# Kernel tuning notes

Hardware: AMD Instinct MI355X
Metric: run time of the kernel (lower is better)

The kernel has to match this reference:

```python
import jax, jax.numpy as jnp
import numpy as np
from math import sqrt

B, S, D, H = 2, 2048, 1024, 16
HD = D // H


def setup_inputs() -> dict:
    key = jax.random.key(0)
    ks = jax.random.split(key, 5)
    std = 0.02
    return {
        "tensor_in": jax.random.normal(ks[0], (B, S, D), dtype=jnp.float32),
        "attention_mask": jnp.zeros((1, 1, S, S), dtype=jnp.float32),
        "Wq": jax.random.normal(ks[1], (D, D), dtype=jnp.float32) * std,
        "Wk": jax.random.normal(ks[2], (D, D), dtype=jnp.float32) * std,
        "Wv": jax.random.normal(ks[3], (D, D), dtype=jnp.float32) * std,
        "Wo": jax.random.normal(ks[4], (D, D), dtype=jnp.float32) * std,
    }


def reference(tensor_in, attention_mask, Wq, Wk, Wv, Wo):
    # nn.Linear(dim, dim, bias=False): y = x @ W.T, W is [out, in]
    q = tensor_in @ Wq.T  # [B,S,D]
    k = tensor_in @ Wk.T
    v = tensor_in @ Wv.T
    # split heads -> [B,H,S,HD]
    q = q.reshape(B, S, H, HD).transpose(0, 2, 1, 3)
    k = k.reshape(B, S, H, HD).transpose(0, 2, 1, 3)
    v = v.reshape(B, S, H, HD).transpose(0, 2, 1, 3)
    # scores [B,H,S,S]; note: mask added BEFORE scaling, scale = sqrt(full dim)
    scores = jnp.einsum("bhqd,bhkd->bhqk", q, k) + attention_mask
    weights = jax.nn.softmax(scores / sqrt(D), axis=-1)  # dropout = identity (eval)
    context = jnp.einsum("bhqk,bhkd->bhqd", weights, v)
    context = context.transpose(0, 2, 1, 3).reshape(B, S, D)
    return context @ Wo.T
```

## Files before the change

kernel.cpp:

```cpp
#include <hip/hip_runtime.h>

#define B_  2
#define S_  2048
#define D_  1024
#define H_  16
#define HD_ 64
#define M_  (B_*S_)

typedef __attribute__((ext_vector_type(8))) short  short8;
typedef __attribute__((ext_vector_type(4))) float  float4v;
typedef __attribute__((ext_vector_type(4))) int    int4v;

#define PSCALE 0.0450843341f

__device__ __forceinline__ unsigned int pack2_bf16(float a, float b) {
#if __has_builtin(__builtin_amdgcn_cvt_pk_bf16_f32)
    auto p = __builtin_amdgcn_cvt_pk_bf16_f32(a, b);
    return __builtin_bit_cast(unsigned int, p);
#else
    unsigned int xa = __builtin_bit_cast(unsigned int, a);
    unsigned int xb = __builtin_bit_cast(unsigned int, b);
    xa += 0x7fffu + ((xa >> 16) & 1u);
    xb += 0x7fffu + ((xb >> 16) & 1u);
    return (xa >> 16) | (xb & 0xffff0000u);
#endif
}
__device__ __forceinline__ unsigned short f_to_bf16bits(float f) {
#if __has_builtin(__builtin_amdgcn_cvt_pk_bf16_f32)
    return (unsigned short)(pack2_bf16(f, f) & 0xffffu);
#else
    unsigned int x = __builtin_bit_cast(unsigned int, f);
    x += 0x7fffu + ((x >> 16) & 1u);
    return (unsigned short)(x >> 16);
#endif
}

__device__ __forceinline__ float fast_exp2(float x) {
#if __has_builtin(__builtin_amdgcn_exp2f)
    return __builtin_amdgcn_exp2f(x);
#else
    return exp2f(x);
#endif
}

__device__ __forceinline__ void async_cp16(const unsigned short* gsrc,
                                           unsigned short* lds_base_uniform) {
#if __has_builtin(__builtin_amdgcn_global_load_lds)
    __builtin_amdgcn_global_load_lds(
        (const __attribute__((address_space(1))) unsigned int*)gsrc,
        (__attribute__((address_space(3))) unsigned int*)lds_base_uniform,
        16, 0, 0);
#else
    const int lane = (int)(threadIdx.x & 63);
    *(int4v*)(lds_base_uniform + lane * 8) = *(const int4v*)gsrc;
#endif
}

__global__ __launch_bounds__(256) void cvt_bf16(
    const float* __restrict__ X,  const float* __restrict__ Wq,
    const float* __restrict__ Wk, const float* __restrict__ Wv,
    const float* __restrict__ Wo,
    unsigned short* __restrict__ Xb,  unsigned short* __restrict__ Wqb,
    unsigned short* __restrict__ Wkb, unsigned short* __restrict__ Wvb,
    unsigned short* __restrict__ Wob)
{
    const long t = (long)blockIdx.x * 256 + threadIdx.x;
    const long e = t * 8;
    const float* src; unsigned short* dst; long off;
    if      (e < 4194304) { src = X;  dst = Xb;  off = e; }
    else if (e < 5242880) { src = Wq; dst = Wqb; off = e - 4194304; }
    else if (e < 6291456) { src = Wk; dst = Wkb; off = e - 5242880; }
    else if (e < 7340032) { src = Wv; dst = Wvb; off = e - 6291456; }
    else                  { src = Wo; dst = Wob; off = e - 7340032; }
    float4v a = *(const float4v*)&src[off];
    float4v b = *(const float4v*)&src[off + 4];
    int4v o;
    o[0] = (int)pack2_bf16(a[0], a[1]);
    o[1] = (int)pack2_bf16(a[2], a[3]);
    o[2] = (int)pack2_bf16(b[0], b[1]);
    o[3] = (int)pack2_bf16(b[2], b[3]);
    *(int4v*)&dst[off] = o;
}

__global__ __launch_bounds__(256) void gemm_bt(
    const unsigned short* __restrict__ A,
    const unsigned short* __restrict__ B0,
    const unsigned short* __restrict__ B1,
    const unsigned short* __restrict__ B2,
    void* __restrict__ O0, void* __restrict__ O1, void* __restrict__ O2,
    int mode_base)
{
    const int K = 1024;
    const int z = blockIdx.z;
    const int mode = mode_base + z;
    const unsigned short* Aop;
    const unsigned short* Bop;
    void* Op = (z == 0) ? O0 : (z == 1) ? O1 : O2;
    int m0, n0;
    if (mode == 2) {
        Aop = B2; Bop = A;
        m0 = blockIdx.y * 128;
        n0 = blockIdx.x * 128;
    } else {
        Aop = A;
        Bop = (z == 0) ? B0 : (z == 1) ? B1 : B2;
        m0 = blockIdx.x * 128;
        n0 = blockIdx.y * 128;
    }

    __shared__ alignas(16) unsigned short As[128 * 64];
    __shared__ alignas(16) unsigned short Bs[128 * 64];

    const int tid  = threadIdx.x;
    const int wv   = tid >> 6;
    const int lane = tid & 63;
    const int wm   = wv >> 1, wn = wv & 1;
    const int q4   = lane >> 4, l15 = lane & 15;

    const unsigned short* gA[4];
    const unsigned short* gB[4];
    unsigned short* ldsA[4];
    unsigned short* ldsB[4];
#pragma unroll
    for (int j = 0; j < 4; j++) {
        const int r = wv * 32 + j * 8 + (lane >> 3);
        const int c = (((lane & 7) ^ (r & 7)) * 8);
        gA[j] = Aop + (long)(m0 + r) * K + c;
        gB[j] = Bop + (long)(n0 + r) * K + c;
        ldsA[j] = &As[(wv * 32 + j * 8) * 64];
        ldsB[j] = &Bs[(wv * 32 + j * 8) * 64];
    }

    int aoff[2][4], boff[2][4];
#pragma unroll
    for (int ks = 0; ks < 2; ks++)
#pragma unroll
        for (int t = 0; t < 4; t++) {
            const int swz = (((ks * 4 + q4) ^ (l15 & 7)) * 8);
            aoff[ks][t] = (wm * 64 + t * 16 + l15) * 64 + swz;
            boff[ks][t] = (wn * 64 + t * 16 + l15) * 64 + swz;
        }

    float4v acc[4][4];
#pragma unroll
    for (int i = 0; i < 4; i++)
#pragma unroll
        for (int j = 0; j < 4; j++) acc[i][j] = (float4v)0.0f;

    for (int k0 = 0; k0 < K; k0 += 64) {
        __syncthreads();
#pragma unroll
        for (int j = 0; j < 4; j++) {
            async_cp16(gA[j], ldsA[j]);
            async_cp16(gB[j], ldsB[j]);
            gA[j] += 64; gB[j] += 64;
        }
        __syncthreads();

#pragma unroll
        for (int ks = 0; ks < 2; ks++) {
            short8 afr[4], bfr[4];
#pragma unroll
            for (int mt = 0; mt < 4; mt++) afr[mt] = *(const short8*)&As[aoff[ks][mt]];
#pragma unroll
            for (int nt = 0; nt < 4; nt++) bfr[nt] = *(const short8*)&Bs[boff[ks][nt]];
#pragma unroll
            for (int mt = 0; mt < 4; mt++)
#pragma unroll
                for (int nt = 0; nt < 4; nt++)
                    acc[mt][nt] = __builtin_amdgcn_mfma_f32_16x16x32_bf16(
                        afr[mt], bfr[nt], acc[mt][nt], 0, 0, 0);
        }
    }

#pragma unroll
    for (int mt = 0; mt < 4; mt++)
#pragma unroll
        for (int nt = 0; nt < 4; nt++)
#pragma unroll
            for (int r = 0; r < 4; r++) {
                const int m = m0 + wm * 64 + mt * 16 + q4 * 4 + r;
                const int n = n0 + wn * 64 + nt * 16 + l15;
                float v = acc[mt][nt][r];
                if (mode == 3) {
                    ((float*)Op)[(long)m * D_ + n] = v;
                } else if (mode == 2) {
                    const long off = (((long)(n >> 11) * H_ + (m >> 6)) * HD_ + (m & 63)) * S_ + (n & 2047);
                    ((unsigned short*)Op)[off] = f_to_bf16bits(v);
                } else {
                    const long off = ((long)((m >> 11) * H_ + (n >> 6)) * S_ + (m & 2047)) * HD_ + (n & 63);
                    if (mode == 0) v *= PSCALE;
                    ((unsigned short*)Op)[off] = f_to_bf16bits(v);
                }
            }
}

__global__ __launch_bounds__(256) void attn(
    const unsigned short* __restrict__ Q,
    const unsigned short* __restrict__ Kk,
    const unsigned short* __restrict__ Vt,
    const float* __restrict__ mask,
    unsigned short* __restrict__ ctx)
{
    __shared__ alignas(16) unsigned short Ks [2][64 * 72];
    __shared__ alignas(16) unsigned short Vts[2][64 * 72];
    __shared__ alignas(16) unsigned short Ps [4][32 * 72];

    const int tid  = threadIdx.x;
    const int wv   = tid >> 6;
    const int lane = tid & 63;
    const int q4   = lane >> 4, l15 = lane & 15;
    const int bh   = blockIdx.y;
    const int q0   = blockIdx.x * 128;

    const long head = (long)bh * S_ * HD_;

    short8 qfr[2][2];
#pragma unroll
    for (int mt = 0; mt < 2; mt++) {
        const int qrow = q0 + wv * 32 + mt * 16 + l15;
        qfr[mt][0] = *(const short8*)&Q[head + (long)qrow * HD_ + q4 * 8];
        qfr[mt][1] = *(const short8*)&Q[head + (long)qrow * HD_ + 32 + q4 * 8];
    }

    float l_acc[2][4];
#pragma unroll
    for (int mt = 0; mt < 2; mt++)
#pragma unroll
        for (int r = 0; r < 4; r++) l_acc[mt][r] = 0.0f;
    float4v oacc[2][4];
#pragma unroll
    for (int mt = 0; mt < 2; mt++)
#pragma unroll
        for (int dt = 0; dt < 4; dt++) oacc[mt][dt] = (float4v)0.0f;

    const int srow = tid >> 3;
    const int scol = (tid & 7) * 8;
    const unsigned short* gK[2];
    const unsigned short* gV[2];
    int ldsOff[2];
#pragma unroll
    for (int j = 0; j < 2; j++) {
        const int row = j * 32 + srow;
        gK[j] = Kk + head + (long)row * HD_ + scol;
        gV[j] = Vt + head + (long)row * S_  + scol;
        ldsOff[j] = row * 72 + scol;
    }

    const float* mrow[2][4];
#pragma unroll
    for (int mt = 0; mt < 2; mt++)
#pragma unroll
        for (int r = 0; r < 4; r++)
            mrow[mt][r] = mask + (long)(q0 + wv * 32 + mt * 16 + q4 * 4 + r) * S_ + l15;

    int4v kreg[2], vreg[2];
#pragma unroll
    for (int j = 0; j < 2; j++) {
        kreg[j] = *(const int4v*)gK[j];
        vreg[j] = *(const int4v*)gV[j];
    }

    for (int it = 0; it < S_ / 64; it++) {
        const int k0  = it * 64;
        const int buf = it & 1;

#pragma unroll
        for (int j = 0; j < 2; j++) {
            *(int4v*)&Ks [buf][ldsOff[j]] = kreg[j];
            *(int4v*)&Vts[buf][ldsOff[j]] = vreg[j];
        }
        __syncthreads();

        if (it + 1 < S_ / 64) {
#pragma unroll
            for (int j = 0; j < 2; j++) {
                kreg[j] = *(const int4v*)(gK[j] + (long)(k0 + 64) * HD_);
                vreg[j] = *(const int4v*)(gV[j] + (k0 + 64));
            }
        }

        float mv[2][4][4];
#pragma unroll
        for (int mt = 0; mt < 2; mt++)
#pragma unroll
            for (int nt = 0; nt < 4; nt++)
#pragma unroll
                for (int r = 0; r < 4; r++)
                    mv[mt][nt][r] = mrow[mt][r][k0 + nt * 16];

        float4v sfr[2][4];
#pragma unroll
        for (int nt = 0; nt < 4; nt++) {
            short8 kb0 = *(const short8*)&Ks[buf][(nt * 16 + l15) * 72 + q4 * 8];
            short8 kb1 = *(const short8*)&Ks[buf][(nt * 16 + l15) * 72 + 32 + q4 * 8];
#pragma unroll
            for (int mt = 0; mt < 2; mt++) {
                float4v s = (float4v)0.0f;
                s = __builtin_amdgcn_mfma_f32_16x16x32_bf16(qfr[mt][0], kb0, s, 0, 0, 0);
                s = __builtin_amdgcn_mfma_f32_16x16x32_bf16(qfr[mt][1], kb1, s, 0, 0, 0);
                sfr[mt][nt] = s;
            }
        }

#pragma unroll
        for (int mt = 0; mt < 2; mt++)
#pragma unroll
            for (int nt = 0; nt < 4; nt++)
#pragma unroll
                for (int r = 0; r < 4; r++) {
                    const float p = fast_exp2(fmaf(mv[mt][nt][r], PSCALE, sfr[mt][nt][r]));
                    l_acc[mt][r] += p;
                    Ps[wv][(mt * 16 + q4 * 4 + r) * 72 + nt * 16 + l15] = f_to_bf16bits(p);
                }

        short8 pf[2][2];
#pragma unroll
        for (int mt = 0; mt < 2; mt++) {
            pf[mt][0] = *(const short8*)&Ps[wv][(mt * 16 + l15) * 72 + q4 * 8];
            pf[mt][1] = *(const short8*)&Ps[wv][(mt * 16 + l15) * 72 + 32 + q4 * 8];
        }

#pragma unroll
        for (int dt = 0; dt < 4; dt++) {
            short8 vb0 = *(const short8*)&Vts[buf][(dt * 16 + l15) * 72 + q4 * 8];
            short8 vb1 = *(const short8*)&Vts[buf][(dt * 16 + l15) * 72 + 32 + q4 * 8];
#pragma unroll
            for (int mt = 0; mt < 2; mt++) {
                float4v o = oacc[mt][dt];
                o = __builtin_amdgcn_mfma_f32_16x16x32_bf16(pf[mt][0], vb0, o, 0, 0, 0);
                o = __builtin_amdgcn_mfma_f32_16x16x32_bf16(pf[mt][1], vb1, o, 0, 0, 0);
                oacc[mt][dt] = o;
            }
        }
    }

#pragma unroll
    for (int mt = 0; mt < 2; mt++)
#pragma unroll
        for (int r = 0; r < 4; r++) {
#pragma unroll
            for (int off = 1; off < 16; off <<= 1)
                l_acc[mt][r] += __shfl_xor(l_acc[mt][r], off);
        }

    const int b = bh >> 4, h = bh & 15;
#pragma unroll
    for (int mt = 0; mt < 2; mt++)
#pragma unroll
        for (int dt = 0; dt < 4; dt++)
#pragma unroll
            for (int r = 0; r < 4; r++) {
                const int qg = q0 + wv * 32 + mt * 16 + q4 * 4 + r;
                const int d  = dt * 16 + l15;
                const float v = oacc[mt][dt][r] / l_acc[mt][r];
                ctx[((long)(b * S_ + qg)) * D_ + h * HD_ + d] = f_to_bf16bits(v);
            }
}

extern "C" void kernel_launch(void* const* d_in, const int* in_sizes, int n_in,
                              void* d_out, int out_size, void* d_ws, size_t ws_size,
                              hipStream_t stream) {
    const float* X    = (const float*)d_in[0];
    const float* mask = (const float*)d_in[1];
    const float* Wq   = (const float*)d_in[2];
    const float* Wk   = (const float*)d_in[3];
    const float* Wv   = (const float*)d_in[4];
    const float* Wo   = (const float*)d_in[5];
    float* out        = (float*)d_out;

    unsigned short* ws = (unsigned short*)d_ws;
    unsigned short* qws  = ws;
    unsigned short* kws  = ws + 4194304;
    unsigned short* vtws = ws + 8388608;
    unsigned short* ctx  = ws + 12582912;
    unsigned short* Xb   = ws + 16777216;
    unsigned short* Wqb  = ws + 20971520;
    unsigned short* Wkb  = ws + 22020096;
    unsigned short* Wvb  = ws + 23068672;
    unsigned short* Wob  = ws + 24117248;

    cvt_bf16<<<dim3(4096), 256, 0, stream>>>(X, Wq, Wk, Wv, Wo, Xb, Wqb, Wkb, Wvb, Wob);
    gemm_bt<<<dim3(32, 8, 3), 256, 0, stream>>>(Xb, Wqb, Wkb, Wvb, qws, kws, vtws, 0);
    attn<<<dim3(16, 32, 1), 256, 0, stream>>>(qws, kws, vtws, mask, ctx);
    gemm_bt<<<dim3(32, 8, 1), 256, 0, stream>>>(ctx, Wob, Wob, Wob, out, out, out, 3);
}
```

Measured before the change: 231.8 us.

## Split attention query tile across eight waves of 16 rows each

The attention kernel now launches 512 threads per block. Each of eight waves owns 16 query rows instead of four waves owning 32 rows. The per-thread K/V staging load drops to one vector per tile and register pressure halves, aiming for higher occupancy and more latency hiding. In exchange each wave reuses every K/V LDS fragment for only one row tile, which doubles LDS reads per MFMA, and block-wide syncs now cover more waves.

```diff
diff --git a/kernel.cpp b/kernel.cpp
--- a/kernel.cpp
+++ b/kernel.cpp
@@ -195,7 +195,7 @@
             }
 }
 
-__global__ __launch_bounds__(256) void attn(
+__global__ __launch_bounds__(512, 4) void attn(
     const unsigned short* __restrict__ Q,
     const unsigned short* __restrict__ Kk,
     const unsigned short* __restrict__ Vt,
@@ -204,7 +204,7 @@
 {
     __shared__ alignas(16) unsigned short Ks [2][64 * 72];
     __shared__ alignas(16) unsigned short Vts[2][64 * 72];
-    __shared__ alignas(16) unsigned short Ps [4][32 * 72];
+    __shared__ alignas(16) unsigned short Ps [8][16 * 72];
 
     const int tid  = threadIdx.x;
     const int wv   = tid >> 6;
@@ -215,147 +215,101 @@
 
     const long head = (long)bh * S_ * HD_;
 
-    short8 qfr[2][2];
-#pragma unroll
-    for (int mt = 0; mt < 2; mt++) {
-        const int qrow = q0 + wv * 32 + mt * 16 + l15;
-        qfr[mt][0] = *(const short8*)&Q[head + (long)qrow * HD_ + q4 * 8];
-        qfr[mt][1] = *(const short8*)&Q[head + (long)qrow * HD_ + 32 + q4 * 8];
-    }
-
-    float l_acc[2][4];
-#pragma unroll
-    for (int mt = 0; mt < 2; mt++)
-#pragma unroll
-        for (int r = 0; r < 4; r++) l_acc[mt][r] = 0.0f;
-    float4v oacc[2][4];
-#pragma unroll
-    for (int mt = 0; mt < 2; mt++)
-#pragma unroll
-        for (int dt = 0; dt < 4; dt++) oacc[mt][dt] = (float4v)0.0f;
+    const int qrow = q0 + wv * 16 + l15;
+    short8 qfr[2];
+    qfr[0] = *(const short8*)&Q[head + (long)qrow * HD_ + q4 * 8];
+    qfr[1] = *(const short8*)&Q[head + (long)qrow * HD_ + 32 + q4 * 8];
+
+    float l_acc[4] = {0.0f, 0.0f, 0.0f, 0.0f};
+    float4v oacc[4];
+#pragma unroll
+    for (int dt = 0; dt < 4; dt++) oacc[dt] = (float4v)0.0f;
 
     const int srow = tid >> 3;
     const int scol = (tid & 7) * 8;
-    const unsigned short* gK[2];
-    const unsigned short* gV[2];
-    int ldsOff[2];
-#pragma unroll
-    for (int j = 0; j < 2; j++) {
-        const int row = j * 32 + srow;
-        gK[j] = Kk + head + (long)row * HD_ + scol;
-        gV[j] = Vt + head + (long)row * S_  + scol;
-        ldsOff[j] = row * 72 + scol;
-    }
-
-    const float* mrow[2][4];
-#pragma unroll
-    for (int mt = 0; mt < 2; mt++)
-#pragma unroll
-        for (int r = 0; r < 4; r++)
-            mrow[mt][r] = mask + (long)(q0 + wv * 32 + mt * 16 + q4 * 4 + r) * S_ + l15;
-
-    int4v kreg[2], vreg[2];
-#pragma unroll
-    for (int j = 0; j < 2; j++) {
-        kreg[j] = *(const int4v*)gK[j];
-        vreg[j] = *(const int4v*)gV[j];
-    }
+    const unsigned short* gK = Kk + head + (long)srow * HD_ + scol;
+    const unsigned short* gV = Vt + head + (long)srow * S_  + scol;
+    const int ldsOff = srow * 72 + scol;
+
+    const float* mrow[4];
+#pragma unroll
+    for (int r = 0; r < 4; r++)
+        mrow[r] = mask + (long)(q0 + wv * 16 + q4 * 4 + r) * S_ + l15;
+
+    int4v kreg = *(const int4v*)gK;
+    int4v vreg = *(const int4v*)gV;
 
     for (int it = 0; it < S_ / 64; it++) {
         const int k0  = it * 64;
         const int buf = it & 1;
 
-#pragma unroll
-        for (int j = 0; j < 2; j++) {
-            *(int4v*)&Ks [buf][ldsOff[j]] = kreg[j];
-            *(int4v*)&Vts[buf][ldsOff[j]] = vreg[j];
-        }
+        *(int4v*)&Ks [buf][ldsOff] = kreg;
+        *(int4v*)&Vts[buf][ldsOff] = vreg;
         __syncthreads();
 
         if (it + 1 < S_ / 64) {
-#pragma unroll
-            for (int j = 0; j < 2; j++) {
-                kreg[j] = *(const int4v*)(gK[j] + (long)(k0 + 64) * HD_);
-                vreg[j] = *(const int4v*)(gV[j] + (k0 + 64));
-            }
-        }
-
-        float mv[2][4][4];
-#pragma unroll
-        for (int mt = 0; mt < 2; mt++)
-#pragma unroll
-            for (int nt = 0; nt < 4; nt++)
-#pragma unroll
-                for (int r = 0; r < 4; r++)
-                    mv[mt][nt][r] = mrow[mt][r][k0 + nt * 16];
-
-        float4v sfr[2][4];
+            kreg = *(const int4v*)(gK + (long)(k0 + 64) * HD_);
+            vreg = *(const int4v*)(gV + (k0 + 64));
+        }
+
+        float mv[4][4];
+#pragma unroll
+        for (int nt = 0; nt < 4; nt++)
+#pragma unroll
+            for (int r = 0; r < 4; r++)
+                mv[nt][r] = mrow[r][k0 + nt * 16];
+
+        float4v sfr[4];
 #pragma unroll
         for (int nt = 0; nt < 4; nt++) {
             short8 kb0 = *(const short8*)&Ks[buf][(nt * 16 + l15) * 72 + q4 * 8];
             short8 kb1 = *(const short8*)&Ks[buf][(nt * 16 + l15) * 72 + 32 + q4 * 8];
-#pragma unroll
-            for (int mt = 0; mt < 2; mt++) {
-                float4v s = (float4v)0.0f;
-                s = __builtin_amdgcn_mfma_f32_16x16x32_bf16(qfr[mt][0], kb0, s, 0, 0, 0);
-                s = __builtin_amdgcn_mfma_f32_16x16x32_bf16(qfr[mt][1], kb1, s, 0, 0, 0);
-                sfr[mt][nt] = s;
+            float4v s = (float4v)0.0f;
+            s = __builtin_amdgcn_mfma_f32_16x16x32_bf16(qfr[0], kb0, s, 0, 0, 0);
+            s = __builtin_amdgcn_mfma_f32_16x16x32_bf16(qfr[1], kb1, s, 0, 0, 0);
+            sfr[nt] = s;
+        }
+
+#pragma unroll
+        for (int nt = 0; nt < 4; nt++)
+#pragma unroll
+            for (int r = 0; r < 4; r++) {
+                const float p = fast_exp2(fmaf(mv[nt][r], PSCALE, sfr[nt][r]));
+                l_acc[r] += p;
+                Ps[wv][(q4 * 4 + r) * 72 + nt * 16 + l15] = f_to_bf16bits(p);
             }
-        }
-
-#pragma unroll
-        for (int mt = 0; mt < 2; mt++)
-#pragma unroll
-            for (int nt = 0; nt < 4; nt++)
-#pragma unroll
-                for (int r = 0; r < 4; r++) {
-                    const float p = fast_exp2(fmaf(mv[mt][nt][r], PSCALE, sfr[mt][nt][r]));
-                    l_acc[mt][r] += p;
-                    Ps[wv][(mt * 16 + q4 * 4 + r) * 72 + nt * 16 + l15] = f_to_bf16bits(p);
-                }
-
-        short8 pf[2][2];
-#pragma unroll
-        for (int mt = 0; mt < 2; mt++) {
-            pf[mt][0] = *(const short8*)&Ps[wv][(mt * 16 + l15) * 72 + q4 * 8];
-            pf[mt][1] = *(const short8*)&Ps[wv][(mt * 16 + l15) * 72 + 32 + q4 * 8];
-        }
+
+        short8 pf0 = *(const short8*)&Ps[wv][l15 * 72 + q4 * 8];
+        short8 pf1 = *(const short8*)&Ps[wv][l15 * 72 + 32 + q4 * 8];
 
 #pragma unroll
         for (int dt = 0; dt < 4; dt++) {
             short8 vb0 = *(const short8*)&Vts[buf][(dt * 16 + l15) * 72 + q4 * 8];
             short8 vb1 = *(const short8*)&Vts[buf][(dt * 16 + l15) * 72 + 32 + q4 * 8];
-#pragma unroll
-            for (int mt = 0; mt < 2; mt++) {
-                float4v o = oacc[mt][dt];
-                o = __builtin_amdgcn_mfma_f32_16x16x32_bf16(pf[mt][0], vb0, o, 0, 0, 0);
-                o = __builtin_amdgcn_mfma_f32_16x16x32_bf16(pf[mt][1], vb1, o, 0, 0, 0);
-                oacc[mt][dt] = o;
-            }
-        }
-    }
-
-#pragma unroll
-    for (int mt = 0; mt < 2; mt++)
+            float4v o = oacc[dt];
+            o = __builtin_amdgcn_mfma_f32_16x16x32_bf16(pf0, vb0, o, 0, 0, 0);
+            o = __builtin_amdgcn_mfma_f32_16x16x32_bf16(pf1, vb1, o, 0, 0, 0);
+            oacc[dt] = o;
+        }
+    }
+
+#pragma unroll
+    for (int r = 0; r < 4; r++) {
+#pragma unroll
+        for (int off = 1; off < 16; off <<= 1)
+            l_acc[r] += __shfl_xor(l_acc[r], off);
+    }
+
+    const int b = bh >> 4, h = bh & 15;
+#pragma unroll
+    for (int dt = 0; dt < 4; dt++)
 #pragma unroll
         for (int r = 0; r < 4; r++) {
-#pragma unroll
-            for (int off = 1; off < 16; off <<= 1)
-                l_acc[mt][r] += __shfl_xor(l_acc[mt][r], off);
-        }
-
-    const int b = bh >> 4, h = bh & 15;
-#pragma unroll
-    for (int mt = 0; mt < 2; mt++)
-#pragma unroll
-        for (int dt = 0; dt < 4; dt++)
-#pragma unroll
-            for (int r = 0; r < 4; r++) {
-                const int qg = q0 + wv * 32 + mt * 16 + q4 * 4 + r;
-                const int d  = dt * 16 + l15;
-                const float v = oacc[mt][dt][r] / l_acc[mt][r];
-                ctx[((long)(b * S_ + qg)) * D_ + h * HD_ + d] = f_to_bf16bits(v);
-            }
+            const int qg = q0 + wv * 16 + q4 * 4 + r;
+            const int d  = dt * 16 + l15;
+            const float v = oacc[dt][r] / l_acc[r];
+            ctx[((long)(b * S_ + qg)) * D_ + h * HD_ + d] = f_to_bf16bits(v);
+        }
 }
 
 extern "C" void kernel_launch(void* const* d_in, const int* in_sizes, int n_in,
@@ -382,6 +336,6 @@
 
     cvt_bf16<<<dim3(4096), 256, 0, stream>>>(X, Wq, Wk, Wv, Wo, Xb, Wqb, Wkb, Wvb, Wob);
     gemm_bt<<<dim3(32, 8, 3), 256, 0, stream>>>(Xb, Wqb, Wkb, Wvb, qws, kws, vtws, 0);
-    attn<<<dim3(16, 32, 1), 256, 0, stream>>>(qws, kws, vtws, mask, ctx);
+    attn<<<dim3(16, 32, 1), 512, 0, stream>>>(qws, kws, vtws, mask, ctx);
     gemm_bt<<<dim3(32, 8, 1), 256, 0, stream>>>(ctx, Wob, Wob, Wob, out, out, out, 3);
 }
```

New measurement: 222.9 us. 3.8% less time.
